# Kernel tuning notes

Hardware: AMD Instinct MI355X
Metric: run time of the kernel (lower is better)

Reference implementation:

```python
import jax, jax.numpy as jnp
import numpy as np
from jax import lax

T_ITERS = 6
LN_EPS = 1e-5

def layer_norm(x, g, b):
    mu = jnp.mean(x, axis=-1, keepdims=True)
    var = jnp.var(x, axis=-1, keepdims=True)
    return (x - mu) * lax.rsqrt(var + LN_EPS) * g + b

def setup_inputs() -> dict:
    key = jax.random.key(0)
    ks = jax.random.split(key, 12)
    B, C_in, S = 8, 128, 33
    hidden = 2 * C_in          # 256
    dim = 256                  # feat_dim
    N = 64
    w = lambda k, shp, s=0.02: (jax.random.normal(k, shp, jnp.float32) * s)
    return {
        "x": jax.random.normal(ks[0], (B, C_in, S, S, S), jnp.float32),
        "templates_init": jax.random.normal(ks[1], (1, N, dim), jnp.float32),
        "conv_w": w(ks[2], (hidden, C_in, 3, 3, 3)),
        "conv_b": jnp.zeros((hidden,), jnp.float32),
        "Wq": w(ks[3], (dim, dim)),
        "Wk": w(ks[4], (hidden, dim)),
        "Wv": w(ks[5], (hidden, dim)),
        "ln_in_g": jnp.ones((hidden,), jnp.float32), "ln_in_b": jnp.zeros((hidden,), jnp.float32),
        "ln_t_g": jnp.ones((dim,), jnp.float32),    "ln_t_b": jnp.zeros((dim,), jnp.float32),
        "ln_m_g": jnp.ones((dim,), jnp.float32),    "ln_m_b": jnp.zeros((dim,), jnp.float32),
        "W1": w(ks[6], (dim, 2 * dim)), "b1": jnp.zeros((2 * dim,), jnp.float32),
        "W2": w(ks[7], (2 * dim, dim)), "b2": jnp.zeros((dim,), jnp.float32),
    }

def reference(x, templates_init, conv_w, conv_b, Wq, Wk, Wv,
              ln_in_g, ln_in_b, ln_t_g, ln_t_b, ln_m_g, ln_m_b,
              W1, b1, W2, b2):
    # project: Conv3d stride 2, no padding, + ReLU
    h = lax.conv_general_dilated(x, conv_w, window_strides=(2, 2, 2),
                                 padding='VALID',
                                 dimension_numbers=('NCDHW', 'OIDHW', 'NCDHW'))
    h = jax.nn.relu(h + conv_b[None, :, None, None, None])
    B, C, X, Y, Z = h.shape
    dim = templates_init.shape[-1]
    N = templates_init.shape[1]
    scale = dim ** (-0.5)
    tokens = h.reshape(B, C, X * Y * Z).transpose(0, 2, 1)   # (B, L, hidden)
    tokens = layer_norm(tokens, ln_in_g, ln_in_b)
    k = tokens @ Wk                                           # (B, L, dim)
    v = tokens @ Wv                                           # (B, L, dim)
    templates = jnp.broadcast_to(templates_init, (B, N, dim))
    attn = None
    for _ in range(T_ITERS):
        t_prev = templates
        t = layer_norm(templates, ln_t_g, ln_t_b)
        q = (t @ Wq) * scale                                  # (B, N, dim)
        attn_logits = jnp.einsum('bnd,bld->bln', q, k)        # (B, L, N)
        attn = jax.nn.softmax(attn_logits, axis=-1)           # competitive over N
        attn = attn + 1e-8
        attn = attn / jnp.sum(attn, axis=-2, keepdims=True)   # renormalize over L
        templates = t_prev + jnp.einsum('bld,bln->bnd', v, attn)
        m = layer_norm(templates, ln_m_g, ln_m_b)
        templates = templates + (jax.nn.gelu(m @ W1 + b1, approximate=False) @ W2 + b2)
    templates_out = templates.transpose(0, 2, 1)              # (B, dim, N)
    attn_out = attn.transpose(0, 2, 1).reshape(B, N, X, Y, Z)
    return templates_out, attn_out
```

## Files before the change

kernel.cpp:

```cpp
#include <hip/hip_runtime.h>

typedef unsigned short u16;
typedef short s16x8 __attribute__((ext_vector_type(8)));
typedef float f32x4 __attribute__((ext_vector_type(4)));
typedef float f32x4u __attribute__((ext_vector_type(4), aligned(4)));
typedef unsigned short us4 __attribute__((ext_vector_type(4)));

__device__ __forceinline__ float bf2f(u16 v) {
    return __uint_as_float(((unsigned int)v) << 16);
}
__device__ __forceinline__ u16 f2bf(float f) {
    unsigned int u = __float_as_uint(f);
    u = u + 0x7FFFu + ((u >> 16) & 1u);
    return (u16)(u >> 16);
}
__device__ __forceinline__ f32x4 mfma16(s16x8 a, s16x8 b, f32x4 c) {
    return __builtin_amdgcn_mfma_f32_16x16x32_bf16(a, b, c, 0, 0, 0);
}
#define ZERO4 f32x4{0.f, 0.f, 0.f, 0.f}

__global__ void prepack_kernel(const float* __restrict__ conv_w, const float* __restrict__ Wk,
                               const float* __restrict__ Wv, const float* __restrict__ Wq,
                               const float* __restrict__ W1, const float* __restrict__ W2,
                               u16* __restrict__ Bp, u16* __restrict__ WkvP, u16* __restrict__ WqP,
                               u16* __restrict__ W1T, u16* __restrict__ W2T)
{
    int idx = blockIdx.x * 256 + threadIdx.x;
    if (idx < 294912) {
        int n = idx / 1152, g = idx - n * 1152;
        int ic = g / 9, r = g - ic * 9;
        const float* s = conv_w + n * 3456 + ic * 27 + r * 3;
        u16* d = Bp + n * 4608 + g * 4;
        d[0] = f2bf(s[0]); d[1] = f2bf(s[1]); d[2] = f2bf(s[2]); d[3] = 0;
    } else if (idx < 425984) {
        int i = idx - 294912;
        int n = i >> 8, c = i & 255;
        WkvP[i] = f2bf((n < 256) ? Wk[c * 256 + n] : Wv[c * 256 + (n - 256)]);
    } else if (idx < 491520) {
        int i = idx - 425984;
        int n = i >> 8, c = i & 255;
        WqP[i] = f2bf(Wq[c * 256 + n]);
    } else if (idx < 622592) {
        int i = idx - 491520;
        int h = i >> 8, c = i & 255;
        W1T[i] = f2bf(W1[c * 512 + h]);
    } else if (idx < 753664) {
        int i = idx - 622592;
        int dd = i >> 9, h = i & 511;
        W2T[i] = f2bf(W2[h * 256 + dd]);
    }
}

__global__ __launch_bounds__(512, 4) void conv_fused(
    const float* __restrict__ x, const u16* __restrict__ Bp, const float* __restrict__ conv_b,
    const float* __restrict__ ln_g, const float* __restrict__ ln_b, const u16* __restrict__ WkvP,
    u16* __restrict__ kbuf, u16* __restrict__ vT)
{
    __shared__ __align__(16) char smem[38400];
    u16* slab   = (u16*)smem;
    u16* tokbf  = (u16*)smem;
    float* lnred  = (float*)(smem + 33792);
    float* lnstat = (float*)(smem + 37888);

    int blk = blockIdx.x;
    int b = blk >> 6, ox = (blk >> 2) & 15, oyb = blk & 3;
    int tid = threadIdx.x, wid = tid >> 6, lane = tid & 63;
    int quad = lane >> 4, l15 = lane & 15;
    int nbase = wid * 32;

    f32x4 acc[4][2];
    #pragma unroll
    for (int i = 0; i < 4; ++i)
        #pragma unroll
        for (int j = 0; j < 2; ++j) acc[i][j] = ZERO4;

    const u16* bprow0 = Bp + (nbase + l15) * 4608 + quad * 8;
    const u16* bprow1 = bprow0 + 16 * 4608;

    for (int icc = 0; icc < 8; ++icc) {
        __syncthreads();
        {
            f32x4u tv[8];
            int so8[8];
            #pragma unroll
            for (int u = 0; u < 8; ++u) {
                int s = tid + u * 512;
                tv[u] = f32x4u{0.f, 0.f, 0.f, 0.f};
                so8[u] = -1;
                if (s < 3888) {
                    int row = s / 9;
                    int c = s - row * 9;
                    int icl = row / 27;
                    int rr = row - icl * 27;
                    int ixl = rr / 9;
                    int iyl = rr - ixl * 9;
                    const float* xr = x + ((size_t)((b * 128 + icc * 16 + icl) * 33)
                                           + (2 * ox + ixl)) * 1089 + (8 * oyb + iyl) * 33;
                    if (c < 8) tv[u] = *(const f32x4u*)(xr + c * 4);
                    else       tv[u].x = xr[32];
                    so8[u] = row * 36 + c * 4;
                }
            }
            #pragma unroll
            for (int u = 0; u < 8; ++u) {
                if (so8[u] >= 0) {
                    us4 w;
                    w.x = f2bf(tv[u].x); w.y = f2bf(tv[u].y);
                    w.z = f2bf(tv[u].z); w.w = f2bf(tv[u].w);
                    *(us4*)(slab + so8[u]) = w;
                }
            }
        }
        __syncthreads();

        const u16* bk0 = bprow0 + icc * 576;
        const u16* bk1 = bprow1 + icc * 576;
        s16x8 bbA[2], bbB[2];
        bbA[0] = *reinterpret_cast<const s16x8*>(bk0);
        bbA[1] = *reinterpret_cast<const s16x8*>(bk1);

#define CONV_STEP(CC, BREG)                                                     \
        {                                                                       \
            int g = (CC) * 8 + quad * 2;                                        \
            int i0 = g / 9, r9 = g - i0 * 9;                                    \
            int kx = r9 / 3, ky = r9 - kx * 3;                                  \
            int base0 = (i0 * 27 + kx * 9 + ky) * 36 + 2 * l15;                 \
            g += 1;                                                             \
            i0 = g / 9; r9 = g - i0 * 9; kx = r9 / 3; ky = r9 - kx * 3;         \
            int base1 = (i0 * 27 + kx * 9 + ky) * 36 + 2 * l15;                 \
            _Pragma("unroll")                                                   \
            for (int fm = 0; fm < 4; ++fm) {                                    \
                union { s16x8 v; ushort2 h[4]; } af;                            \
                const u16* sp0 = slab + base0 + fm * 72;                        \
                const u16* sp1 = slab + base1 + fm * 72;                        \
                af.h[0] = *(const ushort2*)(sp0);                               \
                af.h[1] = *(const ushort2*)(sp0 + 2);                           \
                af.h[2] = *(const ushort2*)(sp1);                               \
                af.h[3] = *(const ushort2*)(sp1 + 2);                           \
                acc[fm][0] = mfma16(af.v, (BREG)[0], acc[fm][0]);               \
                acc[fm][1] = mfma16(af.v, (BREG)[1], acc[fm][1]);               \
            }                                                                   \
        }

        #pragma unroll 1
        for (int c8 = 0; c8 < 18; c8 += 2) {
            bbB[0] = *reinterpret_cast<const s16x8*>(bk0 + (c8 + 1) * 32);
            bbB[1] = *reinterpret_cast<const s16x8*>(bk1 + (c8 + 1) * 32);
            CONV_STEP(c8, bbA)
            if (c8 + 2 < 18) {
                bbA[0] = *reinterpret_cast<const s16x8*>(bk0 + (c8 + 2) * 32);
                bbA[1] = *reinterpret_cast<const s16x8*>(bk1 + (c8 + 2) * 32);
            }
            CONV_STEP(c8 + 1, bbB)
        }
#undef CONV_STEP
    }
    #pragma unroll
    for (int fn = 0; fn < 2; ++fn) {
        float bias = conv_b[nbase + fn * 16 + l15];
        #pragma unroll
        for (int fm = 0; fm < 4; ++fm)
            #pragma unroll
            for (int r = 0; r < 4; ++r)
                acc[fm][fn][r] = fmaxf(acc[fm][fn][r] + bias, 0.f);
    }
    #pragma unroll
    for (int fm = 0; fm < 4; ++fm) {
        #pragma unroll
        for (int r = 0; r < 4; ++r) {
            float s = acc[fm][0][r] + acc[fm][1][r];
            float q2 = acc[fm][0][r] * acc[fm][0][r] + acc[fm][1][r] * acc[fm][1][r];
            #pragma unroll
            for (int msk = 1; msk <= 8; msk <<= 1) {
                s  += __shfl_xor(s, msk, 64);
                q2 += __shfl_xor(q2, msk, 64);
            }
            if (l15 == 0) {
                int mm = fm * 16 + quad * 4 + r;
                lnred[(wid * 64 + mm) * 2 + 0] = s;
                lnred[(wid * 64 + mm) * 2 + 1] = q2;
            }
        }
    }
    __syncthreads();
    if (tid < 64) {
        float s = 0, q2 = 0;
        #pragma unroll
        for (int w = 0; w < 8; ++w) { s += lnred[(w * 64 + tid) * 2]; q2 += lnred[(w * 64 + tid) * 2 + 1]; }
        float mu = s * (1.f / 256.f);
        float var = fmaxf(q2 * (1.f / 256.f) - mu * mu, 0.f);
        lnstat[tid * 2]     = mu;
        lnstat[tid * 2 + 1] = rsqrtf(var + 1e-5f);
    }
    __syncthreads();
    {
        float gam[2], bet[2];
        #pragma unroll
        for (int fn = 0; fn < 2; ++fn) {
            int n = nbase + fn * 16 + l15;
            gam[fn] = ln_g[n]; bet[fn] = ln_b[n];
        }
        #pragma unroll
        for (int fm = 0; fm < 4; ++fm)
            #pragma unroll
            for (int r = 0; r < 4; ++r) {
                int mm = fm * 16 + quad * 4 + r;
                float mu = lnstat[mm * 2], rs = lnstat[mm * 2 + 1];
                #pragma unroll
                for (int fn = 0; fn < 2; ++fn) {
                    int n = nbase + fn * 16 + l15;
                    tokbf[mm * 264 + n] = f2bf((acc[fm][fn][r] - mu) * rs * gam[fn] + bet[fn]);
                }
            }
    }
    __syncthreads();
    f32x4 kacc[4][4];
    #pragma unroll
    for (int i = 0; i < 4; ++i)
        #pragma unroll
        for (int j = 0; j < 4; ++j) kacc[i][j] = ZERO4;
    int n2 = wid * 64;
    const u16* wp = WkvP + (n2 + l15) * 256 + quad * 8;
    s16x8 wvA[4], wvB[4];
    #pragma unroll
    for (int fn = 0; fn < 4; ++fn) wvA[fn] = *reinterpret_cast<const s16x8*>(wp + fn * 4096);

#define KV_STEP(KK, WREG)                                                           \
    {                                                                               \
        s16x8 a2[4];                                                                \
        _Pragma("unroll")                                                           \
        for (int fm = 0; fm < 4; ++fm)                                              \
            a2[fm] = *reinterpret_cast<const s16x8*>(tokbf + (fm * 16 + l15) * 264  \
                                                     + (KK) * 32 + quad * 8);       \
        _Pragma("unroll")                                                           \
        for (int fn = 0; fn < 4; ++fn)                                              \
            _Pragma("unroll")                                                       \
            for (int fm = 0; fm < 4; ++fm)                                          \
                kacc[fm][fn] = mfma16(a2[fm], (WREG)[fn], kacc[fm][fn]);            \
    }

    #pragma unroll 1
    for (int kc = 0; kc < 8; kc += 2) {
        #pragma unroll
        for (int fn = 0; fn < 4; ++fn)
            wvB[fn] = *reinterpret_cast<const s16x8*>(wp + fn * 4096 + (kc + 1) * 32);
        KV_STEP(kc, wvA)
        if (kc + 2 < 8) {
            #pragma unroll
            for (int fn = 0; fn < 4; ++fn)
                wvA[fn] = *reinterpret_cast<const s16x8*>(wp + fn * 4096 + (kc + 2) * 32);
        }
        KV_STEP(kc + 1, wvB)
    }
#undef KV_STEP

    #pragma unroll
    for (int fm = 0; fm < 4; ++fm)
        #pragma unroll
        for (int r = 0; r < 4; ++r) {
            int l = (ox * 16 + oyb * 4 + fm) * 16 + quad * 4 + r;
            #pragma unroll
            for (int fn = 0; fn < 4; ++fn) {
                int n = n2 + fn * 16 + l15;
                u16 v = f2bf(kacc[fm][fn][r]);
                if (n < 256) kbuf[((b << 12) + l) * 256 + n] = v;
                else         vT[((b * 256 + (n - 256)) << 12) + l] = v;
            }
        }
}

__global__ __launch_bounds__(256) void kQ(
    const float* __restrict__ tinit, float* __restrict__ tpl,
    const float* __restrict__ ln_t_g, const float* __restrict__ ln_t_b,
    const u16* __restrict__ WqP, u16* __restrict__ qbuf,
    float* __restrict__ colsum, float* __restrict__ delta)
{
    __shared__ __align__(16) u16 mls[64 * 264];
    __shared__ float pls[64][4][2];
    __shared__ float stat[64][2];
    int b = blockIdx.x, tid = threadIdx.x;
    int m = tid >> 2, part = tid & 3;
    const float* tp = tinit + m * 256 + part * 64;
    float* tg = tpl + (b * 64 + m) * 256 + part * 64;
    float s = 0, q2 = 0;
    for (int i = 0; i < 64; ++i) {
        float v = tp[i];
        tg[i] = v;
        s += v; q2 += v * v;
    }
    pls[m][part][0] = s; pls[m][part][1] = q2;
    __syncthreads();
    if (tid < 64) {
        float ss = 0, qq = 0;
        #pragma unroll
        for (int p = 0; p < 4; ++p) { ss += pls[tid][p][0]; qq += pls[tid][p][1]; }
        float mu = ss * (1.f / 256.f);
        float var = fmaxf(qq * (1.f / 256.f) - mu * mu, 0.f);
        stat[tid][0] = mu; stat[tid][1] = rsqrtf(var + 1e-5f);
    }
    __syncthreads();
    {
        float mu = stat[m][0], rs = stat[m][1];
        for (int i = 0; i < 64; ++i) {
            int d = part * 64 + i;
            mls[m * 264 + d] = f2bf((tp[i] - mu) * rs * ln_t_g[d] + ln_t_b[d]);
        }
    }
    __syncthreads();
    int wid = tid >> 6, lane = tid & 63, quad = lane >> 4, l15 = lane & 15;
    f32x4 qa[4][4];
    #pragma unroll
    for (int i = 0; i < 4; ++i)
        #pragma unroll
        for (int j = 0; j < 4; ++j) qa[i][j] = ZERO4;
    #pragma unroll 1
    for (int kc = 0; kc < 8; ++kc) {
        s16x8 a[4];
        #pragma unroll
        for (int fm = 0; fm < 4; ++fm)
            a[fm] = *reinterpret_cast<const s16x8*>(mls + (fm * 16 + l15) * 264 + kc * 32 + quad * 8);
        #pragma unroll
        for (int fn = 0; fn < 4; ++fn) {
            s16x8 bv = *reinterpret_cast<const s16x8*>(WqP + (wid * 64 + fn * 16 + l15) * 256 + kc * 32 + quad * 8);
            #pragma unroll
            for (int fm = 0; fm < 4; ++fm)
                qa[fm][fn] = mfma16(a[fm], bv, qa[fm][fn]);
        }
    }
    #pragma unroll
    for (int fm = 0; fm < 4; ++fm)
        #pragma unroll
        for (int fn = 0; fn < 4; ++fn)
            #pragma unroll
            for (int r = 0; r < 4; ++r) {
                int mt = fm * 16 + quad * 4 + r;
                int d = wid * 64 + fn * 16 + l15;
                qbuf[(b * 64 + mt) * 256 + d] = f2bf(qa[fm][fn][r] * 0.0625f);
            }
    if (tid < 64) colsum[b * 64 + tid] = 0.f;
    f32x4* dz = (f32x4*)(delta + b * 16384);
    for (int i = tid; i < 4096; i += 256) dz[i] = ZERO4;
}

__global__ __launch_bounds__(256) void kP(
    const u16* __restrict__ qbuf, const u16* __restrict__ kbuf, const u16* __restrict__ vT,
    float* __restrict__ colsum, float* __restrict__ delta, int last, u16* __restrict__ attnT)
{
    __shared__ __align__(16) u16 atile[64 * 264];
    int b = blockIdx.x >> 4, ltg = blockIdx.x & 15;
    int tid = threadIdx.x, wid = tid >> 6, lane = tid & 63;
    int quad = lane >> 4, l15 = lane & 15;
    const u16* qb = qbuf + b * 16384;
    float colp[4] = {0.f, 0.f, 0.f, 0.f};
    #pragma unroll 1
    for (int rt = 0; rt < 4; ++rt) {
        int lrow = ltg * 256 + wid * 64 + rt * 16;
        const u16* arow = kbuf + ((b << 12) + lrow + l15) * 256;
        f32x4 sa[4];
        #pragma unroll
        for (int fn = 0; fn < 4; ++fn) sa[fn] = ZERO4;
        #pragma unroll 1
        for (int kc = 0; kc < 8; ++kc) {
            s16x8 a = *reinterpret_cast<const s16x8*>(arow + kc * 32 + quad * 8);
            #pragma unroll
            for (int fn = 0; fn < 4; ++fn) {
                s16x8 bv = *reinterpret_cast<const s16x8*>(qb + (fn * 16 + l15) * 256 + kc * 32 + quad * 8);
                sa[fn] = mfma16(a, bv, sa[fn]);
            }
        }
        #pragma unroll
        for (int r = 0; r < 4; ++r) {
            float mx = fmaxf(fmaxf(sa[0][r], sa[1][r]), fmaxf(sa[2][r], sa[3][r]));
            #pragma unroll
            for (int msk = 1; msk <= 8; msk <<= 1) mx = fmaxf(mx, __shfl_xor(mx, msk, 64));
            float e[4], sum = 0;
            #pragma unroll
            for (int fn = 0; fn < 4; ++fn) { e[fn] = __expf(sa[fn][r] - mx); sum += e[fn]; }
            #pragma unroll
            for (int msk = 1; msk <= 8; msk <<= 1) sum += __shfl_xor(sum, msk, 64);
            float inv = 1.f / sum;
            #pragma unroll
            for (int fn = 0; fn < 4; ++fn) {
                float p = e[fn] * inv + 1e-8f;
                colp[fn] += p;
                atile[(fn * 16 + l15) * 264 + wid * 64 + rt * 16 + quad * 4 + r] = f2bf(p);
            }
        }
    }
    #pragma unroll
    for (int fn = 0; fn < 4; ++fn) {
        float c = colp[fn];
        c += __shfl_xor(c, 16, 64);
        c += __shfl_xor(c, 32, 64);
        colp[fn] = c;
    }
    if (lane < 16) {
        #pragma unroll
        for (int fn = 0; fn < 4; ++fn)
            atomicAdd(&colsum[b * 64 + fn * 16 + lane], colp[fn]);
    }
    __syncthreads();
    f32x4 acc[4][4];
    #pragma unroll
    for (int i = 0; i < 4; ++i)
        #pragma unroll
        for (int j = 0; j < 4; ++j) acc[i][j] = ZERO4;
    #pragma unroll 1
    for (int kc = 0; kc < 8; ++kc) {
        s16x8 a[4];
        #pragma unroll
        for (int fm = 0; fm < 4; ++fm)
            a[fm] = *reinterpret_cast<const s16x8*>(atile + (fm * 16 + l15) * 264 + kc * 32 + quad * 8);
        #pragma unroll
        for (int fn = 0; fn < 4; ++fn) {
            s16x8 bv = *reinterpret_cast<const s16x8*>(
                vT + ((b * 256 + wid * 64 + fn * 16 + l15) << 12) + ltg * 256 + kc * 32 + quad * 8);
            #pragma unroll
            for (int fm = 0; fm < 4; ++fm)
                acc[fm][fn] = mfma16(a[fm], bv, acc[fm][fn]);
        }
    }
    #pragma unroll
    for (int fm = 0; fm < 4; ++fm)
        #pragma unroll
        for (int fn = 0; fn < 4; ++fn)
            #pragma unroll
            for (int r = 0; r < 4; ++r) {
                int nt = fm * 16 + quad * 4 + r;
                int d = wid * 64 + fn * 16 + l15;
                atomicAdd(&delta[(b * 64 + nt) * 256 + d], acc[fm][fn][r]);
            }
    if (last) {
        int n = tid >> 2, lo = (tid & 3) * 64;
        const u16* src = atile + n * 264 + lo;
        u16* dst = attnT + ((b * 64 + n) << 12) + ltg * 256 + lo;
        #pragma unroll
        for (int j = 0; j < 8; ++j)
            *(int4*)(dst + j * 8) = *(const int4*)(src + j * 8);
    }
}

__global__ __launch_bounds__(256) void kT(
    float* __restrict__ tpl, const float* __restrict__ delta, float* __restrict__ colsum,
    const float* __restrict__ ln_m_g, const float* __restrict__ ln_m_b,
    const u16* __restrict__ W1T, const float* __restrict__ b1,
    const u16* __restrict__ W2T, const float* __restrict__ b2,
    const float* __restrict__ ln_t_g, const float* __restrict__ ln_t_b,
    const u16* __restrict__ WqP, u16* __restrict__ qbuf,
    float* __restrict__ deltaz, int last, float* __restrict__ out0)
{
    __shared__ __align__(16) u16 mls[16 * 264];
    __shared__ __align__(16) u16 hid[16 * 520];
    __shared__ float pls[16][16][2];
    __shared__ float stat[16][2];
    __shared__ float lnr2[4][16][2];
    int b = blockIdx.x >> 2, mg = blockIdx.x & 3;
    int m0 = mg * 16;
    int tid = threadIdx.x, wid = tid >> 6, lane = tid & 63;
    int quad = lane >> 4, l15 = lane & 15;
    {
        int ml = tid >> 4, part = tid & 15;
        float cinv = 1.f / colsum[b * 64 + m0 + ml];
        float* tg = tpl + (b * 64 + m0 + ml) * 256 + part * 16;
        const float* dg = delta + (b * 64 + m0 + ml) * 256 + part * 16;
        float vbuf[16];
        float s = 0, q2 = 0;
        #pragma unroll
        for (int i = 0; i < 16; ++i) {
            float v = tg[i] + dg[i] * cinv;
            vbuf[i] = v; s += v; q2 += v * v;
        }
        pls[ml][part][0] = s; pls[ml][part][1] = q2;
        __syncthreads();
        if (tid < 16) {
            float ss = 0, qq = 0;
            #pragma unroll
            for (int p = 0; p < 16; ++p) { ss += pls[tid][p][0]; qq += pls[tid][p][1]; }
            float mu = ss * (1.f / 256.f);
            float var = fmaxf(qq * (1.f / 256.f) - mu * mu, 0.f);
            stat[tid][0] = mu; stat[tid][1] = rsqrtf(var + 1e-5f);
        }
        __syncthreads();
        float mu = stat[ml][0], rs = stat[ml][1];
        #pragma unroll
        for (int i = 0; i < 16; ++i) {
            int d = part * 16 + i;
            tg[i] = vbuf[i];
            mls[ml * 264 + d] = f2bf((vbuf[i] - mu) * rs * ln_m_g[d] + ln_m_b[d]);
        }
    }
    __syncthreads();
    {
        f32x4 ha[8];
        #pragma unroll
        for (int j = 0; j < 8; ++j) ha[j] = ZERO4;
        #pragma unroll 1
        for (int kc = 0; kc < 8; ++kc) {
            s16x8 a = *reinterpret_cast<const s16x8*>(mls + l15 * 264 + kc * 32 + quad * 8);
            #pragma unroll
            for (int fn = 0; fn < 8; ++fn) {
                s16x8 bv = *reinterpret_cast<const s16x8*>(W1T + (wid * 128 + fn * 16 + l15) * 256 + kc * 32 + quad * 8);
                ha[fn] = mfma16(a, bv, ha[fn]);
            }
        }
        #pragma unroll
        for (int fn = 0; fn < 8; ++fn) {
            int nh = wid * 128 + fn * 16 + l15;
            float bb = b1[nh];
            #pragma unroll
            for (int r = 0; r < 4; ++r) {
                float v = ha[fn][r] + bb;
                v = 0.5f * v * (1.f + erff(v * 0.70710678118654752f));
                hid[(quad * 4 + r) * 520 + nh] = f2bf(v);
            }
        }
    }
    __syncthreads();
    {
        f32x4 oa[4];
        #pragma unroll
        for (int j = 0; j < 4; ++j) oa[j] = ZERO4;
        #pragma unroll 1
        for (int kc = 0; kc < 16; ++kc) {
            s16x8 a = *reinterpret_cast<const s16x8*>(hid + l15 * 520 + kc * 32 + quad * 8);
            #pragma unroll
            for (int fn = 0; fn < 4; ++fn) {
                s16x8 bv = *reinterpret_cast<const s16x8*>(W2T + (wid * 64 + fn * 16 + l15) * 512 + kc * 32 + quad * 8);
                oa[fn] = mfma16(a, bv, oa[fn]);
            }
        }
        #pragma unroll
        for (int fn = 0; fn < 4; ++fn) {
            int d = wid * 64 + fn * 16 + l15;
            float bb = b2[d];
            #pragma unroll
            for (int r = 0; r < 4; ++r) {
                int mm = quad * 4 + r;
                oa[fn][r] += bb + tpl[(b * 64 + m0 + mm) * 256 + d];
            }
        }
        #pragma unroll
        for (int r = 0; r < 4; ++r) {
            float s = oa[0][r] + oa[1][r] + oa[2][r] + oa[3][r];
            float q2 = oa[0][r] * oa[0][r] + oa[1][r] * oa[1][r]
                     + oa[2][r] * oa[2][r] + oa[3][r] * oa[3][r];
            #pragma unroll
            for (int msk = 1; msk <= 8; msk <<= 1) {
                s  += __shfl_xor(s, msk, 64);
                q2 += __shfl_xor(q2, msk, 64);
            }
            if (l15 == 0) {
                lnr2[wid][quad * 4 + r][0] = s;
                lnr2[wid][quad * 4 + r][1] = q2;
            }
        }
        __syncthreads();
        if (tid < 16) {
            float ss = 0, qq = 0;
            #pragma unroll
            for (int w = 0; w < 4; ++w) { ss += lnr2[w][tid][0]; qq += lnr2[w][tid][1]; }
            float mu = ss * (1.f / 256.f);
            float var = fmaxf(qq * (1.f / 256.f) - mu * mu, 0.f);
            stat[tid][0] = mu; stat[tid][1] = rsqrtf(var + 1e-5f);
        }
        __syncthreads();
        #pragma unroll
        for (int fn = 0; fn < 4; ++fn) {
            int d = wid * 64 + fn * 16 + l15;
            float gg = last ? 0.f : ln_t_g[d];
            float bt = last ? 0.f : ln_t_b[d];
            #pragma unroll
            for (int r = 0; r < 4; ++r) {
                int mm = quad * 4 + r;
                float v = oa[fn][r];
                tpl[(b * 64 + m0 + mm) * 256 + d] = v;
                if (last) {
                    out0[(b * 256 + d) * 64 + m0 + mm] = v;
                } else {
                    mls[mm * 264 + d] = f2bf((v - stat[mm][0]) * stat[mm][1] * gg + bt);
                }
            }
        }
    }
    if (!last) {
        __syncthreads();
        f32x4 qa[4];
        #pragma unroll
        for (int j = 0; j < 4; ++j) qa[j] = ZERO4;
        #pragma unroll 1
        for (int kc = 0; kc < 8; ++kc) {
            s16x8 a = *reinterpret_cast<const s16x8*>(mls + l15 * 264 + kc * 32 + quad * 8);
            #pragma unroll
            for (int fn = 0; fn < 4; ++fn) {
                s16x8 bv = *reinterpret_cast<const s16x8*>(WqP + (wid * 64 + fn * 16 + l15) * 256 + kc * 32 + quad * 8);
                qa[fn] = mfma16(a, bv, qa[fn]);
            }
        }
        #pragma unroll
        for (int fn = 0; fn < 4; ++fn)
            #pragma unroll
            for (int r = 0; r < 4; ++r) {
                int mt = m0 + quad * 4 + r;
                int d = wid * 64 + fn * 16 + l15;
                qbuf[(b * 64 + mt) * 256 + d] = f2bf(qa[fn][r] * 0.0625f);
            }
        if (tid < 16) colsum[b * 64 + m0 + tid] = 0.f;
        f32x4* dz = (f32x4*)(deltaz + (b * 64 + m0) * 256);
        for (int i = tid; i < 1024; i += 256) dz[i] = ZERO4;
    }
}

__global__ void kE(const u16* __restrict__ attnT, const float* __restrict__ colsum,
                   float* __restrict__ out1)
{
    int idx = blockIdx.x * 256 + threadIdx.x;
    int e = idx * 4;
    int b = e >> 18, n = (e >> 12) & 63;
    float ci = 1.f / colsum[b * 64 + n];
    const u16* s = attnT + e;
    f32x4 o;
    o.x = bf2f(s[0]) * ci; o.y = bf2f(s[1]) * ci;
    o.z = bf2f(s[2]) * ci; o.w = bf2f(s[3]) * ci;
    *(f32x4*)(out1 + e) = o;
}

extern "C" void kernel_launch(void* const* d_in, const int* in_sizes, int n_in,
                              void* d_out, int out_size, void* d_ws, size_t ws_size,
                              hipStream_t stream)
{
    const float* x       = (const float*)d_in[0];
    const float* tinit   = (const float*)d_in[1];
    const float* conv_w  = (const float*)d_in[2];
    const float* conv_b  = (const float*)d_in[3];
    const float* Wq      = (const float*)d_in[4];
    const float* Wk      = (const float*)d_in[5];
    const float* Wv      = (const float*)d_in[6];
    const float* ln_in_g = (const float*)d_in[7];
    const float* ln_in_b = (const float*)d_in[8];
    const float* ln_t_g  = (const float*)d_in[9];
    const float* ln_t_b  = (const float*)d_in[10];
    const float* ln_m_g  = (const float*)d_in[11];
    const float* ln_m_b  = (const float*)d_in[12];
    const float* W1      = (const float*)d_in[13];
    const float* b1      = (const float*)d_in[14];
    const float* W2      = (const float*)d_in[15];
    const float* b2      = (const float*)d_in[16];

    char* ws = (char*)d_ws;
    u16* Bp       = (u16*)(ws + 0);
    u16* WkvP     = (u16*)(ws + 2359296);
    u16* WqP      = (u16*)(ws + 2621440);
    u16* W1T      = (u16*)(ws + 2752512);
    u16* W2T      = (u16*)(ws + 3014656);
    u16* kbuf     = (u16*)(ws + 3276800);
    u16* vT       = (u16*)(ws + 20054016);
    u16* qbuf     = (u16*)(ws + 36831232);
    u16* attnT    = (u16*)(ws + 37093376);
    float* colsum = (float*)(ws + 41287680);
    float* tpl    = (float*)(ws + 41289728);
    float* delta  = (float*)(ws + 41814016);

    float* out0 = (float*)d_out;
    float* out1 = out0 + 131072;

    prepack_kernel<<<2944, 256, 0, stream>>>(conv_w, Wk, Wv, Wq, W1, W2, Bp, WkvP, WqP, W1T, W2T);
    conv_fused<<<512, 512, 0, stream>>>(x, Bp, conv_b, ln_in_g, ln_in_b, WkvP, kbuf, vT);
    kQ<<<8, 256, 0, stream>>>(tinit, tpl, ln_t_g, ln_t_b, WqP, qbuf, colsum, delta);
    for (int it = 0; it < 6; ++it) {
        int last = (it == 5) ? 1 : 0;
        kP<<<128, 256, 0, stream>>>(qbuf, kbuf, vT, colsum, delta, last, attnT);
        kT<<<32, 256, 0, stream>>>(tpl, delta, colsum, ln_m_g, ln_m_b, W1T, b1, W2T, b2,
                                   ln_t_g, ln_t_b, WqP, qbuf, delta, last, out0);
    }
    kE<<<2048, 256, 0, stream>>>(attnT, colsum, out1);
}
```

Baseline: 816.1 us.

## Split attention into softmax and PV kernels, replacing atomics with partial sums

The fused softmax+PV kernel becomes two kernels. kP computes logits and softmax over 256 blocks of 512 threads, writes bf16 attention to global memory every iteration, and stores per-block column partial sums. A new kPV kernel computes attn·V with one block per (batch, 16-column d tile), reduces across waves in shared memory, and writes delta directly instead of using float atomics. This removes atomic contention and the zeroing of delta and colsum, and raises parallelism. In exchange it adds an extra launch per iteration and a global round trip of the attention matrix.

```diff
diff --git a/kernel.cpp b/kernel.cpp
--- a/kernel.cpp
+++ b/kernel.cpp
@@ -272,8 +272,7 @@
 __global__ __launch_bounds__(256) void kQ(
     const float* __restrict__ tinit, float* __restrict__ tpl,
     const float* __restrict__ ln_t_g, const float* __restrict__ ln_t_b,
-    const u16* __restrict__ WqP, u16* __restrict__ qbuf,
-    float* __restrict__ colsum, float* __restrict__ delta)
+    const u16* __restrict__ WqP, u16* __restrict__ qbuf)
 {
     __shared__ __align__(16) u16 mls[64 * 264];
     __shared__ float pls[64][4][2];
@@ -337,54 +336,49 @@
                 int d = wid * 64 + fn * 16 + l15;
                 qbuf[(b * 64 + mt) * 256 + d] = f2bf(qa[fm][fn][r] * 0.0625f);
             }
-    if (tid < 64) colsum[b * 64 + tid] = 0.f;
-    f32x4* dz = (f32x4*)(delta + b * 16384);
-    for (int i = tid; i < 4096; i += 256) dz[i] = ZERO4;
-}
-
-__global__ __launch_bounds__(256) void kP(
-    const u16* __restrict__ qbuf, const u16* __restrict__ kbuf, const u16* __restrict__ vT,
-    float* __restrict__ colsum, float* __restrict__ delta, int last, u16* __restrict__ attnT)
-{
-    __shared__ __align__(16) u16 atile[64 * 264];
-    int b = blockIdx.x >> 4, ltg = blockIdx.x & 15;
+}
+
+__global__ __launch_bounds__(512, 2) void kP(
+    const u16* __restrict__ qbuf, const u16* __restrict__ kbuf,
+    float* __restrict__ cs_part, u16* __restrict__ attnT)
+{
+    __shared__ __align__(16) u16 atile[64 * 136];
+    __shared__ float colsh[8][64];
+    int b = blockIdx.x >> 5, ltg = blockIdx.x & 31;
     int tid = threadIdx.x, wid = tid >> 6, lane = tid & 63;
     int quad = lane >> 4, l15 = lane & 15;
     const u16* qb = qbuf + b * 16384;
+    int lrow = ltg * 128 + wid * 16;
+    const u16* arow = kbuf + (size_t)((b << 12) + lrow + l15) * 256;
+    f32x4 sa[4];
+    #pragma unroll
+    for (int fn = 0; fn < 4; ++fn) sa[fn] = ZERO4;
+    #pragma unroll 1
+    for (int kc = 0; kc < 8; ++kc) {
+        s16x8 a = *reinterpret_cast<const s16x8*>(arow + kc * 32 + quad * 8);
+        #pragma unroll
+        for (int fn = 0; fn < 4; ++fn) {
+            s16x8 bv = *reinterpret_cast<const s16x8*>(qb + (fn * 16 + l15) * 256 + kc * 32 + quad * 8);
+            sa[fn] = mfma16(a, bv, sa[fn]);
+        }
+    }
     float colp[4] = {0.f, 0.f, 0.f, 0.f};
-    #pragma unroll 1
-    for (int rt = 0; rt < 4; ++rt) {
-        int lrow = ltg * 256 + wid * 64 + rt * 16;
-        const u16* arow = kbuf + ((b << 12) + lrow + l15) * 256;
-        f32x4 sa[4];
-        #pragma unroll
-        for (int fn = 0; fn < 4; ++fn) sa[fn] = ZERO4;
-        #pragma unroll 1
-        for (int kc = 0; kc < 8; ++kc) {
-            s16x8 a = *reinterpret_cast<const s16x8*>(arow + kc * 32 + quad * 8);
-            #pragma unroll
-            for (int fn = 0; fn < 4; ++fn) {
-                s16x8 bv = *reinterpret_cast<const s16x8*>(qb + (fn * 16 + l15) * 256 + kc * 32 + quad * 8);
-                sa[fn] = mfma16(a, bv, sa[fn]);
-            }
-        }
-        #pragma unroll
-        for (int r = 0; r < 4; ++r) {
-            float mx = fmaxf(fmaxf(sa[0][r], sa[1][r]), fmaxf(sa[2][r], sa[3][r]));
-            #pragma unroll
-            for (int msk = 1; msk <= 8; msk <<= 1) mx = fmaxf(mx, __shfl_xor(mx, msk, 64));
-            float e[4], sum = 0;
-            #pragma unroll
-            for (int fn = 0; fn < 4; ++fn) { e[fn] = __expf(sa[fn][r] - mx); sum += e[fn]; }
-            #pragma unroll
-            for (int msk = 1; msk <= 8; msk <<= 1) sum += __shfl_xor(sum, msk, 64);
-            float inv = 1.f / sum;
-            #pragma unroll
-            for (int fn = 0; fn < 4; ++fn) {
-                float p = e[fn] * inv + 1e-8f;
-                colp[fn] += p;
-                atile[(fn * 16 + l15) * 264 + wid * 64 + rt * 16 + quad * 4 + r] = f2bf(p);
-            }
+    #pragma unroll
+    for (int r = 0; r < 4; ++r) {
+        float mx = fmaxf(fmaxf(sa[0][r], sa[1][r]), fmaxf(sa[2][r], sa[3][r]));
+        #pragma unroll
+        for (int msk = 1; msk <= 8; msk <<= 1) mx = fmaxf(mx, __shfl_xor(mx, msk, 64));
+        float e[4], sum = 0;
+        #pragma unroll
+        for (int fn = 0; fn < 4; ++fn) { e[fn] = __expf(sa[fn][r] - mx); sum += e[fn]; }
+        #pragma unroll
+        for (int msk = 1; msk <= 8; msk <<= 1) sum += __shfl_xor(sum, msk, 64);
+        float inv = 1.f / sum;
+        #pragma unroll
+        for (int fn = 0; fn < 4; ++fn) {
+            float p = e[fn] * inv + 1e-8f;
+            colp[fn] += p;
+            atile[(fn * 16 + l15) * 136 + wid * 16 + quad * 4 + r] = f2bf(p);
         }
     }
     #pragma unroll
@@ -392,75 +386,91 @@
         float c = colp[fn];
         c += __shfl_xor(c, 16, 64);
         c += __shfl_xor(c, 32, 64);
-        colp[fn] = c;
-    }
-    if (lane < 16) {
-        #pragma unroll
-        for (int fn = 0; fn < 4; ++fn)
-            atomicAdd(&colsum[b * 64 + fn * 16 + lane], colp[fn]);
-    }
-    __syncthreads();
-    f32x4 acc[4][4];
-    #pragma unroll
-    for (int i = 0; i < 4; ++i)
-        #pragma unroll
-        for (int j = 0; j < 4; ++j) acc[i][j] = ZERO4;
+        if (lane < 16) colsh[wid][fn * 16 + lane] = c;
+    }
+    __syncthreads();
+    if (tid < 64) {
+        float s = 0;
+        #pragma unroll
+        for (int w = 0; w < 8; ++w) s += colsh[w][tid];
+        cs_part[((b << 5) + ltg) * 64 + tid] = s;
+    }
+    {
+        int n = tid >> 3, lo = (tid & 7) * 16;
+        const u16* src = atile + n * 136 + lo;
+        u16* dst = attnT + (size_t)((b * 64 + n) << 12) + ltg * 128 + lo;
+        *(int4*)(dst)     = *(const int4*)(src);
+        *(int4*)(dst + 8) = *(const int4*)(src + 8);
+    }
+}
+
+__global__ __launch_bounds__(512, 2) void kPV(
+    const u16* __restrict__ attnT, const u16* __restrict__ vT, float* __restrict__ delta)
+{
+    __shared__ float pred[8][64][16];
+    int b = blockIdx.x >> 4, dt = blockIdx.x & 15;
+    int tid = threadIdx.x, wid = tid >> 6, lane = tid & 63;
+    int quad = lane >> 4, l15 = lane & 15;
+    const u16* prow = attnT + (size_t)((b * 64 + l15) << 12) + wid * 512 + quad * 8;
+    const u16* vrow = vT + (size_t)((b * 256 + dt * 16 + l15) << 12) + wid * 512 + quad * 8;
+    f32x4 acc[4];
+    #pragma unroll
+    for (int i = 0; i < 4; ++i) acc[i] = ZERO4;
     #pragma unroll 1
-    for (int kc = 0; kc < 8; ++kc) {
-        s16x8 a[4];
-        #pragma unroll
-        for (int fm = 0; fm < 4; ++fm)
-            a[fm] = *reinterpret_cast<const s16x8*>(atile + (fm * 16 + l15) * 264 + kc * 32 + quad * 8);
-        #pragma unroll
-        for (int fn = 0; fn < 4; ++fn) {
-            s16x8 bv = *reinterpret_cast<const s16x8*>(
-                vT + ((b * 256 + wid * 64 + fn * 16 + l15) << 12) + ltg * 256 + kc * 32 + quad * 8);
-            #pragma unroll
-            for (int fm = 0; fm < 4; ++fm)
-                acc[fm][fn] = mfma16(a[fm], bv, acc[fm][fn]);
+    for (int kc = 0; kc < 16; ++kc) {
+        s16x8 bv = *reinterpret_cast<const s16x8*>(vrow + kc * 32);
+        #pragma unroll
+        for (int fm = 0; fm < 4; ++fm) {
+            s16x8 a = *reinterpret_cast<const s16x8*>(prow + (fm << 16) + kc * 32);
+            acc[fm] = mfma16(a, bv, acc[fm]);
         }
     }
     #pragma unroll
     for (int fm = 0; fm < 4; ++fm)
         #pragma unroll
-        for (int fn = 0; fn < 4; ++fn)
-            #pragma unroll
-            for (int r = 0; r < 4; ++r) {
-                int nt = fm * 16 + quad * 4 + r;
-                int d = wid * 64 + fn * 16 + l15;
-                atomicAdd(&delta[(b * 64 + nt) * 256 + d], acc[fm][fn][r]);
-            }
-    if (last) {
-        int n = tid >> 2, lo = (tid & 3) * 64;
-        const u16* src = atile + n * 264 + lo;
-        u16* dst = attnT + ((b * 64 + n) << 12) + ltg * 256 + lo;
-        #pragma unroll
-        for (int j = 0; j < 8; ++j)
-            *(int4*)(dst + j * 8) = *(const int4*)(src + j * 8);
+        for (int r = 0; r < 4; ++r)
+            pred[wid][fm * 16 + quad * 4 + r][l15] = acc[fm][r];
+    __syncthreads();
+    for (int i = tid; i < 1024; i += 512) {
+        int n = i >> 4, d = i & 15;
+        float s = 0;
+        #pragma unroll
+        for (int w = 0; w < 8; ++w) s += pred[w][n][d];
+        delta[(size_t)(b * 64 + n) * 256 + dt * 16 + d] = s;
     }
 }
 
 __global__ __launch_bounds__(256) void kT(
-    float* __restrict__ tpl, const float* __restrict__ delta, float* __restrict__ colsum,
+    float* __restrict__ tpl, const float* __restrict__ delta, const float* __restrict__ cs_part,
+    float* __restrict__ colsum,
     const float* __restrict__ ln_m_g, const float* __restrict__ ln_m_b,
     const u16* __restrict__ W1T, const float* __restrict__ b1,
     const u16* __restrict__ W2T, const float* __restrict__ b2,
     const float* __restrict__ ln_t_g, const float* __restrict__ ln_t_b,
     const u16* __restrict__ WqP, u16* __restrict__ qbuf,
-    float* __restrict__ deltaz, int last, float* __restrict__ out0)
+    int last, float* __restrict__ out0)
 {
     __shared__ __align__(16) u16 mls[16 * 264];
     __shared__ __align__(16) u16 hid[16 * 520];
     __shared__ float pls[16][16][2];
     __shared__ float stat[16][2];
     __shared__ float lnr2[4][16][2];
+    __shared__ float csh[16];
     int b = blockIdx.x >> 2, mg = blockIdx.x & 3;
     int m0 = mg * 16;
     int tid = threadIdx.x, wid = tid >> 6, lane = tid & 63;
     int quad = lane >> 4, l15 = lane & 15;
+    if (tid < 16) {
+        float s = 0;
+        #pragma unroll
+        for (int g = 0; g < 32; ++g) s += cs_part[((b << 5) + g) * 64 + m0 + tid];
+        csh[tid] = 1.f / s;
+        if (last) colsum[b * 64 + m0 + tid] = s;
+    }
+    __syncthreads();
     {
         int ml = tid >> 4, part = tid & 15;
-        float cinv = 1.f / colsum[b * 64 + m0 + ml];
+        float cinv = csh[ml];
         float* tg = tpl + (b * 64 + m0 + ml) * 256 + part * 16;
         const float* dg = delta + (b * 64 + m0 + ml) * 256 + part * 16;
         float vbuf[16];
@@ -604,9 +614,6 @@
                 int d = wid * 64 + fn * 16 + l15;
                 qbuf[(b * 64 + mt) * 256 + d] = f2bf(qa[fn][r] * 0.0625f);
             }
-        if (tid < 16) colsum[b * 64 + m0 + tid] = 0.f;
-        f32x4* dz = (f32x4*)(deltaz + (b * 64 + m0) * 256);
-        for (int i = tid; i < 1024; i += 256) dz[i] = ZERO4;
     }
 }
 
@@ -659,18 +666,20 @@
     float* colsum = (float*)(ws + 41287680);
     float* tpl    = (float*)(ws + 41289728);
     float* delta  = (float*)(ws + 41814016);
+    float* cs_part= (float*)(ws + 42338304);
 
     float* out0 = (float*)d_out;
     float* out1 = out0 + 131072;
 
     prepack_kernel<<<2944, 256, 0, stream>>>(conv_w, Wk, Wv, Wq, W1, W2, Bp, WkvP, WqP, W1T, W2T);
     conv_fused<<<512, 512, 0, stream>>>(x, Bp, conv_b, ln_in_g, ln_in_b, WkvP, kbuf, vT);
-    kQ<<<8, 256, 0, stream>>>(tinit, tpl, ln_t_g, ln_t_b, WqP, qbuf, colsum, delta);
+    kQ<<<8, 256, 0, stream>>>(tinit, tpl, ln_t_g, ln_t_b, WqP, qbuf);
     for (int it = 0; it < 6; ++it) {
         int last = (it == 5) ? 1 : 0;
-        kP<<<128, 256, 0, stream>>>(qbuf, kbuf, vT, colsum, delta, last, attnT);
-        kT<<<32, 256, 0, stream>>>(tpl, delta, colsum, ln_m_g, ln_m_b, W1T, b1, W2T, b2,
-                                   ln_t_g, ln_t_b, WqP, qbuf, delta, last, out0);
+        kP<<<256, 512, 0, stream>>>(qbuf, kbuf, cs_part, attnT);
+        kPV<<<128, 512, 0, stream>>>(attnT, vT, delta);
+        kT<<<32, 256, 0, stream>>>(tpl, delta, cs_part, colsum, ln_m_g, ln_m_b, W1T, b1, W2T, b2,
+                                   ln_t_g, ln_t_b, WqP, qbuf, last, out0);
     }
     kE<<<2048, 256, 0, stream>>>(attnT, colsum, out1);
 }
```

Measured after the change: 820.7 us. No clear change (+0.6%).
